# Optimization experiments

Hardware: AMD Instinct MI355X
Metric: run time of the kernel (lower is better)

Reference implementation:

```python
import jax, jax.numpy as jnp
import numpy as np

N_NODES = 50000
N_EDGES = 800000
D_NODE = 128
D_EDGE = 16
HID = 64
EPS = 1e-5


def _sage_conv(x, src, dst, Wl, bl, Wr, n_nodes):
    # PyG SAGEConv (mean aggr): out = lin_l(mean_{src->dst} x[src]) + lin_r(x)
    msg = x[src]                                        # [E, F] gather
    s = jax.ops.segment_sum(msg, dst, num_segments=n_nodes)   # [N, F]
    cnt = jax.ops.segment_sum(jnp.ones((src.shape[0],), x.dtype), dst,
                              num_segments=n_nodes)
    agg = s / jnp.maximum(cnt, 1.0)[:, None]
    return agg @ Wl.T + bl + x @ Wr.T


def _batchnorm(h, gamma, beta):
    # training-mode BN over node dim (biased variance, as in torch)
    mu = jnp.mean(h, axis=0)
    var = jnp.mean((h - mu) ** 2, axis=0)
    return gamma * (h - mu) / jnp.sqrt(var + EPS) + beta


def setup_inputs() -> dict:
    key = jax.random.key(0)
    ks = jax.random.split(key, 16)
    def lin(k, out_f, in_f):
        lim = 1.0 / np.sqrt(in_f)
        return jax.random.uniform(k, (out_f, in_f), jnp.float32, -lim, lim)
    x = jax.random.normal(ks[0], (N_NODES, D_NODE), jnp.float32)
    edge_index = jax.random.randint(ks[1], (2, N_EDGES), 0, N_NODES, jnp.int64)
    edge_attr = jax.random.normal(ks[2], (N_EDGES, D_EDGE), jnp.float32)
    return {
        "x": x, "edge_index": edge_index, "edge_attr": edge_attr,
        # SAGEConv 1
        "W1l": lin(ks[3], HID, D_NODE), "b1l": jnp.zeros((HID,), jnp.float32),
        "W1r": lin(ks[4], HID, D_NODE),
        "g1": jnp.ones((HID,), jnp.float32), "be1": jnp.zeros((HID,), jnp.float32),
        # SAGEConv 2
        "W2l": lin(ks[5], HID, HID), "b2l": jnp.zeros((HID,), jnp.float32),
        "W2r": lin(ks[6], HID, HID),
        "g2": jnp.ones((HID,), jnp.float32), "be2": jnp.zeros((HID,), jnp.float32),
        # edge MLP: (2*HID + D_EDGE) -> 128 -> 64 -> 2
        "Wm1": lin(ks[7], 128, 2 * HID + D_EDGE), "bm1": jnp.zeros((128,), jnp.float32),
        "Wm2": lin(ks[8], 64, 128), "bm2": jnp.zeros((64,), jnp.float32),
        "Wm3": lin(ks[9], 2, 64), "bm3": jnp.zeros((2,), jnp.float32),
    }


def reference(x, edge_index, edge_attr,
              W1l, b1l, W1r, g1, be1,
              W2l, b2l, W2r, g2, be2,
              Wm1, bm1, Wm2, bm2, Wm3, bm3):
    src, dst = edge_index[0], edge_index[1]
    n = x.shape[0]
    h = _sage_conv(x, src, dst, W1l, b1l, W1r, n)
    h = jax.nn.relu(_batchnorm(h, g1, be1))          # dropout = identity (eval)
    h = _sage_conv(h, src, dst, W2l, b2l, W2r, n)
    h = jax.nn.relu(_batchnorm(h, g2, be2))
    edge_in = jnp.concatenate([h[src], edge_attr, h[dst]], axis=1)  # [E, 144]
    z = jax.nn.relu(edge_in @ Wm1.T + bm1)
    z = jax.nn.relu(z @ Wm2.T + bm2)
    return z @ Wm3.T + bm3                           # [E, 2] logits
```

## Files before the change

### kernel.cpp

```cpp
#include <hip/hip_runtime.h>
#include <hip/hip_fp16.h>


#define EPS 1e-5f

typedef _Float16 h8 __attribute__((ext_vector_type(8)));
typedef float f32x4 __attribute__((ext_vector_type(4)));

__global__ __launch_bounds__(256) void k_prep_hist(
    const float* __restrict__ W1l, const float* __restrict__ W1r,
    const float* __restrict__ b1l,
    const float* __restrict__ W2l, const float* __restrict__ W2r,
    const float* __restrict__ b2l,
    const float* __restrict__ Wm1, const float* __restrict__ Wm2,
    float* __restrict__ Wt1, float* __restrict__ Wt2,
    float* __restrict__ bias1, float* __restrict__ bias2,
    __half* __restrict__ W2B, __half* __restrict__ W1B,
    const int* __restrict__ dst, int* __restrict__ deg, int E, int prepBlocks) {
  if ((int)blockIdx.x >= prepBlocks) {
    int e = (blockIdx.x - prepBlocks) * 256 + threadIdx.x;
    if (e < E) atomicAdd(&deg[dst[e]], 1);
    return;
  }
  int idx = blockIdx.x * 256 + threadIdx.x;
  if (idx < 16384) {
    int k = idx >> 7, f = idx & 127;
    Wt1[idx] = (f < 64) ? W1l[f * 128 + k] : W1r[(f - 64) * 128 + k];
    return;
  }
  idx -= 16384;
  if (idx < 8192) {
    int k = idx >> 7, f = idx & 127;
    Wt2[idx] = (f < 64) ? W2l[f * 64 + k] : W2r[(f - 64) * 64 + k];
    return;
  }
  idx -= 8192;
  if (idx < 128) { bias1[idx] = (idx < 64) ? 0.f : b1l[idx - 64]; return; }
  idx -= 128;
  if (idx < 128) { bias2[idx] = (idx < 64) ? 0.f : b2l[idx - 64]; return; }
  idx -= 128;
  if (idx < 8192) {
    int j = idx & 7, l = (idx >> 3) & 63, f = idx >> 9;
    int kc = f >> 2, tt = f & 3;
    int col = 16 * tt + (l & 15);
    int k = 32 * kc + (l >> 4) * 8 + j;
    W2B[idx] = __float2half(Wm2[col * 128 + k]);
    return;
  }
  idx -= 8192;
  if (idx < 20480) {
    int j = idx & 7, l = (idx >> 3) & 63, f = idx >> 9;
    int kc = f >> 3, nc = f & 7;
    int k = 32 * kc + (l >> 4) * 8 + j;
    int n = 16 * nc + (l & 15);
    float w;
    if (k < 64)       w = Wm1[n * 144 + k];
    else if (k < 128) w = Wm1[n * 144 + 80 + (k - 64)];
    else if (k < 144) w = Wm1[n * 144 + 64 + (k - 128)];
    else              w = 0.f;
    W1B[idx] = __float2half(w);
    return;
  }
}

__global__ __launch_bounds__(1024) void k_scan(
    const int* __restrict__ deg, int* __restrict__ rowptr,
    int* __restrict__ cursor, int N) {
  __shared__ int wsum[16];
  __shared__ int carry;
  const int lane = threadIdx.x & 63;
  const int w    = threadIdx.x >> 6;
  if (threadIdx.x == 0) carry = 0;
  __syncthreads();
  for (int base = 0; base < N; base += 1024) {
    int i = base + threadIdx.x;
    int v = (i < N) ? deg[i] : 0;
    int incl = v;
#pragma unroll
    for (int off = 1; off < 64; off <<= 1) {
      int t = __shfl_up(incl, off);
      if (lane >= off) incl += t;
    }
    if (lane == 63) wsum[w] = incl;
    __syncthreads();
    if (w == 0) {
      int ws_ = (lane < 16) ? wsum[lane] : 0;
      int wincl = ws_;
#pragma unroll
      for (int off = 1; off < 16; off <<= 1) {
        int t = __shfl_up(wincl, off);
        if (lane >= off) wincl += t;
      }
      if (lane < 16) wsum[lane] = wincl;
    }
    __syncthreads();
    int woff = carry + (w > 0 ? wsum[w - 1] : 0);
    int excl = woff + incl - v;
    if (i < N) { rowptr[i] = excl; cursor[i] = excl; }
    int tot = wsum[15];
    __syncthreads();
    if (threadIdx.x == 0) carry += tot;
    __syncthreads();
  }
  if (threadIdx.x == 0) rowptr[N] = carry;
}

__global__ __launch_bounds__(256) void k_fill(
    const int* __restrict__ src, const int* __restrict__ dst,
    int* __restrict__ cursor, int* __restrict__ csr_src,
    int* __restrict__ csr_dst, int* __restrict__ csr_eid,
    int* __restrict__ pos, int E) {
  int e = blockIdx.x * 256 + threadIdx.x;
  if (e < E) {
    int d = dst[e];
    int p = atomicAdd(&cursor[d], 1);
    csr_src[p] = src[e];
    csr_dst[p] = d;
    csr_eid[p] = e;
    pos[e] = p;
  }
}

__global__ __launch_bounds__(256) void k_scatter_out(
    const float* __restrict__ out2, const int* __restrict__ pos,
    float* __restrict__ out, int E) {
  int e = blockIdx.x * 256 + threadIdx.x;
  if (e < E) {
    int p = pos[e];
    *(float2*)&out[(size_t)e * 2] = *(const float2*)&out2[(size_t)p * 2];
  }
}

template<int K, int MODE>
__global__ __launch_bounds__(256) void k_gemm(
    const float* __restrict__ X, const float* __restrict__ stats,
    const float* __restrict__ Wt, const float* __restrict__ bias,
    __half* __restrict__ outH, float* __restrict__ outF, int N, int Ftot) {
  __shared__ __align__(16) float Xs[32][68];
  __shared__ __align__(16) float Ws_[32][128];
  const int tid = threadIdx.x;
  const int tx  = tid & 15;
  const int ty  = tid >> 4;
  const int n0  = blockIdx.x * 64;
  float acc[4][8];
#pragma unroll
  for (int j = 0; j < 8; ++j) {
    float bv = bias[8 * tx + j];
#pragma unroll
    for (int i = 0; i < 4; ++i) acc[i][j] = bv;
  }
  for (int k0 = 0; k0 < K; k0 += 32) {
    __syncthreads();
#pragma unroll
    for (int l = 0; l < 2; ++l) {
      int idx = tid * 2 + l;
      int kq = idx & 7, n = idx >> 3;
      float4 xv = make_float4(0.f, 0.f, 0.f, 0.f);
      if (n0 + n < N) xv = *(const float4*)&X[(size_t)(n0 + n) * K + k0 + kq * 4];
      if (stats) {
        int kb = k0 + kq * 4;
        xv.x = fmaxf(xv.x * stats[128 + kb + 0] + stats[192 + kb + 0], 0.f);
        xv.y = fmaxf(xv.y * stats[128 + kb + 1] + stats[192 + kb + 1], 0.f);
        xv.z = fmaxf(xv.z * stats[128 + kb + 2] + stats[192 + kb + 2], 0.f);
        xv.w = fmaxf(xv.w * stats[128 + kb + 3] + stats[192 + kb + 3], 0.f);
      }
      Xs[kq * 4 + 0][n] = xv.x;
      Xs[kq * 4 + 1][n] = xv.y;
      Xs[kq * 4 + 2][n] = xv.z;
      Xs[kq * 4 + 3][n] = xv.w;
    }
#pragma unroll
    for (int l = 0; l < 4; ++l) {
      int idx = tid + l * 256;
      int kr = idx >> 5, fc = idx & 31;
      *(float4*)&Ws_[kr][fc * 4] =
          *(const float4*)&Wt[(size_t)(k0 + kr) * Ftot + fc * 4];
    }
    __syncthreads();
#pragma unroll
    for (int kk = 0; kk < 32; ++kk) {
      float4 a  = *(const float4*)&Xs[kk][4 * ty];
      float4 b0 = *(const float4*)&Ws_[kk][8 * tx];
      float4 b1 = *(const float4*)&Ws_[kk][8 * tx + 4];
      float aa[4] = {a.x, a.y, a.z, a.w};
      float bb[8] = {b0.x, b0.y, b0.z, b0.w, b1.x, b1.y, b1.z, b1.w};
#pragma unroll
      for (int i = 0; i < 4; ++i)
#pragma unroll
        for (int j = 0; j < 8; ++j) acc[i][j] += aa[i] * bb[j];
    }
  }
#pragma unroll
  for (int i = 0; i < 4; ++i) {
    int n = n0 + 4 * ty + i;
    if (n >= N) continue;
    if (tx < 8) {
      __half2 hh[4];
#pragma unroll
      for (int c = 0; c < 4; ++c)
        hh[c] = __floats2half2_rn(acc[i][2 * c], acc[i][2 * c + 1]);
      *(uint4*)&outH[(size_t)n * 64 + 8 * tx] = *(uint4*)hh;
    } else {
      float* cp = outF + (size_t)n * 64 + 8 * tx - 64;
      *(float4*)cp = make_float4(acc[i][0], acc[i][1], acc[i][2], acc[i][3]);
      *(float4*)(cp + 4) = make_float4(acc[i][4], acc[i][5], acc[i][6], acc[i][7]);
    }
  }
}

__global__ __launch_bounds__(256) void k_agg(
    const __half* __restrict__ qb, const float* __restrict__ pb,
    const int* __restrict__ rowptr, const int* __restrict__ csr_src,
    float* __restrict__ hpre, float* __restrict__ stats, int N) {
  __shared__ float red[512];
  const int tid  = threadIdx.x;
  const int w    = tid >> 6;
  const int lane = tid & 63;
  const int g    = lane >> 3, c = lane & 7;
  float lsum = 0.f, lsq = 0.f;
  const int wid = blockIdx.x * 4 + w;
  const int nw  = gridDim.x * 4;
  for (int n = wid; n < N; n += nw) {
    const int r0 = rowptr[n], r1 = rowptr[n + 1];
    float s[8] = {0.f, 0.f, 0.f, 0.f, 0.f, 0.f, 0.f, 0.f};
    for (int j = r0 + g; j < r1; j += 8) {
      int a = csr_src[j];
      uint4 rv = *(const uint4*)&qb[(size_t)a * 64 + 8 * c];
      const __half2* hp = (const __half2*)&rv;
#pragma unroll
      for (int q = 0; q < 4; ++q) {
        float2 f2 = __half22float2(hp[q]);
        s[2 * q]     += f2.x;
        s[2 * q + 1] += f2.y;
      }
    }
#pragma unroll
    for (int m = 8; m < 64; m <<= 1)
#pragma unroll
      for (int q = 0; q < 8; ++q) s[q] += __shfl_xor(s[q], m);
    float sv = s[0];
#pragma unroll
    for (int q = 1; q < 8; ++q) sv = (g == q) ? s[q] : sv;
    float cdeg = (float)(r1 - r0);
    cdeg = cdeg > 1.f ? cdeg : 1.f;
    const int f = 8 * c + g;
    float v = sv / cdeg + pb[(size_t)n * 64 + f];
    hpre[(size_t)n * 64 + f] = v;
    lsum += v;
    lsq  += v * v;
  }
  red[tid]       = lsum;
  red[256 + tid] = lsq;
  __syncthreads();
  if (tid < 64) {
    float ts = red[tid] + red[tid + 64] + red[tid + 128] + red[tid + 192];
    float tq = red[256 + tid] + red[256 + tid + 64] + red[256 + tid + 128] + red[256 + tid + 192];
    int f = 8 * (tid & 7) + (tid >> 3);
    atomicAdd(&stats[f], ts);
    atomicAdd(&stats[64 + f], tq);
  }
}

__global__ void k_finalize(float* stats, const float* __restrict__ g,
                           const float* __restrict__ be, int N) {
  int f = threadIdx.x;
  float inv_n = 1.0f / (float)N;
  float mean = stats[f] * inv_n;
  float var  = stats[64 + f] * inv_n - mean * mean;
  float s = g[f] * rsqrtf(var + EPS);
  stats[128 + f] = s;
  stats[192 + f] = be[f] - mean * s;
}

__global__ __launch_bounds__(256) void k_bn(
    const float* __restrict__ H1, const float* __restrict__ stats,
    __half* __restrict__ H2, int N) {
  int idx = blockIdx.x * 256 + threadIdx.x;
  if (idx >= N * 8) return;
  int n = idx >> 3, f8 = (idx & 7) * 8;
  float4 h0 = *(const float4*)&H1[(size_t)n * 64 + f8];
  float4 h1 = *(const float4*)&H1[(size_t)n * 64 + f8 + 4];
  const float* sc = stats + 128 + f8;
  const float* sh = stats + 192 + f8;
  __half2 hh[4];
  hh[0] = __floats2half2_rn(fmaxf(h0.x * sc[0] + sh[0], 0.f),
                            fmaxf(h0.y * sc[1] + sh[1], 0.f));
  hh[1] = __floats2half2_rn(fmaxf(h0.z * sc[2] + sh[2], 0.f),
                            fmaxf(h0.w * sc[3] + sh[3], 0.f));
  hh[2] = __floats2half2_rn(fmaxf(h1.x * sc[4] + sh[4], 0.f),
                            fmaxf(h1.y * sc[5] + sh[5], 0.f));
  hh[3] = __floats2half2_rn(fmaxf(h1.z * sc[6] + sh[6], 0.f),
                            fmaxf(h1.w * sc[7] + sh[7], 0.f));
  *(uint4*)&H2[(size_t)n * 64 + f8] = *(uint4*)hh;
}

__global__ __launch_bounds__(256, 2) void k_edge(
    const __half* __restrict__ H2, const float* __restrict__ attr,
    const int* __restrict__ csrc, const int* __restrict__ cdst,
    const int* __restrict__ ceid,
    const __half* __restrict__ W1Bws, const __half* __restrict__ W2Bws,
    const float* __restrict__ bm1, const float* __restrict__ bm2,
    const float* __restrict__ Wm3, const float* __restrict__ bm3,
    float* __restrict__ out2, int E) {
  __shared__ __align__(16) _Float16 W1B[20480];
  __shared__ __align__(16) _Float16 W2B[8192];
  __shared__ __align__(16) _Float16 Z1f[64 * 136];

  const int tid  = threadIdx.x;
  const int lane = tid & 63;
  const int w    = tid >> 6;
  const int ln15 = lane & 15;
  const int quad = lane >> 4;

  for (int i = tid; i < 2560; i += 256)
    ((uint4*)W1B)[i] = ((const uint4*)W1Bws)[i];
  for (int i = tid; i < 1024; i += 256)
    ((uint4*)W2B)[i] = ((const uint4*)W2Bws)[i];

  float bm1v[8];
#pragma unroll
  for (int nc = 0; nc < 8; ++nc) bm1v[nc] = bm1[16 * nc + ln15];
  float bmv[4], w30[4], w31[4];
#pragma unroll
  for (int t = 0; t < 4; ++t) {
    bmv[t] = bm2[16 * t + ln15];
    w30[t] = Wm3[16 * t + ln15];
    w31[t] = Wm3[64 + 16 * t + ln15];
  }
  const float bm30 = bm3[0], bm31 = bm3[1];
  __syncthreads();

  const int nt = (E + 63) >> 6;
  const int G  = gridDim.x;
  const int rowoff = 16 * w + ln15;
  const int t0 = blockIdx.x;

#define ATTR_FRAG(EID, AF)                                                   \
  {                                                                          \
    AF = (h8){0, 0, 0, 0, 0, 0, 0, 0};                                       \
    if (quad < 2) {                                                          \
      float4 f0_ = *(const float4*)&attr[(size_t)(EID) * 16 + 8 * quad];     \
      float4 f1_ = *(const float4*)&attr[(size_t)(EID) * 16 + 8 * quad + 4]; \
      AF[0] = (_Float16)f0_.x; AF[1] = (_Float16)f0_.y;                      \
      AF[2] = (_Float16)f0_.z; AF[3] = (_Float16)f0_.w;                      \
      AF[4] = (_Float16)f1_.x; AF[5] = (_Float16)f1_.y;                      \
      AF[6] = (_Float16)f1_.z; AF[7] = (_Float16)f1_.w;                      \
    }                                                                        \
  }

  int s1, d1, e1i;
  h8 af0, af1, af2, af3, af4;
  {
    int er = (t0 << 6) + rowoff;
    if (er >= E) er = E - 1;
    int s = csrc[er], d = cdst[er], ei_ = ceid[er];
    af0 = *(const h8*)&H2[(size_t)s * 64 + 8 * quad];
    af1 = *(const h8*)&H2[(size_t)s * 64 + 32 + 8 * quad];
    af2 = *(const h8*)&H2[(size_t)d * 64 + 8 * quad];
    af3 = *(const h8*)&H2[(size_t)d * 64 + 32 + 8 * quad];
    ATTR_FRAG(ei_, af4);
  }
  {
    int er = ((t0 + G) << 6) + rowoff;
    if (er >= E) er = E - 1;
    s1 = csrc[er]; d1 = cdst[er]; e1i = ceid[er];
  }

  for (int t = t0; t < nt; t += G) {
    h8 nf0 = *(const h8*)&H2[(size_t)s1 * 64 + 8 * quad];
    h8 nf1 = *(const h8*)&H2[(size_t)s1 * 64 + 32 + 8 * quad];
    h8 nf2 = *(const h8*)&H2[(size_t)d1 * 64 + 8 * quad];
    h8 nf3 = *(const h8*)&H2[(size_t)d1 * 64 + 32 + 8 * quad];

    f32x4 acc1[8];
#pragma unroll
    for (int nc = 0; nc < 8; ++nc)
      acc1[nc] = (f32x4){bm1v[nc], bm1v[nc], bm1v[nc], bm1v[nc]};
#pragma unroll
    for (int nc = 0; nc < 8; ++nc)
      acc1[nc] = __builtin_amdgcn_mfma_f32_16x16x32_f16(
          af0, *(const h8*)&W1B[((0 * 8 + nc) << 9) + (lane << 3)], acc1[nc], 0, 0, 0);
#pragma unroll
    for (int nc = 0; nc < 8; ++nc)
      acc1[nc] = __builtin_amdgcn_mfma_f32_16x16x32_f16(
          af1, *(const h8*)&W1B[((1 * 8 + nc) << 9) + (lane << 3)], acc1[nc], 0, 0, 0);
#pragma unroll
    for (int nc = 0; nc < 8; ++nc)
      acc1[nc] = __builtin_amdgcn_mfma_f32_16x16x32_f16(
          af2, *(const h8*)&W1B[((2 * 8 + nc) << 9) + (lane << 3)], acc1[nc], 0, 0, 0);
#pragma unroll
    for (int nc = 0; nc < 8; ++nc)
      acc1[nc] = __builtin_amdgcn_mfma_f32_16x16x32_f16(
          af3, *(const h8*)&W1B[((3 * 8 + nc) << 9) + (lane << 3)], acc1[nc], 0, 0, 0);
#pragma unroll
    for (int nc = 0; nc < 8; ++nc)
      acc1[nc] = __builtin_amdgcn_mfma_f32_16x16x32_f16(
          af4, *(const h8*)&W1B[((4 * 8 + nc) << 9) + (lane << 3)], acc1[nc], 0, 0, 0);

    h8 nf4;
    ATTR_FRAG(e1i, nf4);
    int s2, d2, e2i;
    {
      int er = ((t + 2 * G) << 6) + rowoff;
      if (er >= E) er = E - 1;
      s2 = csrc[er]; d2 = cdst[er]; e2i = ceid[er];
    }

    const int ebase = 16 * w + 4 * quad;
#pragma unroll
    for (int nc = 0; nc < 8; ++nc)
#pragma unroll
      for (int r = 0; r < 4; ++r)
        Z1f[(ebase + r) * 136 + 16 * nc + ln15] =
            (_Float16)fmaxf(acc1[nc][r], 0.f);

    f32x4 acc2[4];
#pragma unroll
    for (int tt = 0; tt < 4; ++tt)
      acc2[tt] = (f32x4){bmv[tt], bmv[tt], bmv[tt], bmv[tt]};
#pragma unroll
    for (int kc = 0; kc < 4; ++kc) {
      h8 a = *(const h8*)&Z1f[(16 * w + ln15) * 136 + 32 * kc + 8 * quad];
#pragma unroll
      for (int tt = 0; tt < 4; ++tt) {
        h8 bf = *(const h8*)&W2B[((kc * 4 + tt) * 64 + lane) * 8];
        acc2[tt] = __builtin_amdgcn_mfma_f32_16x16x32_f16(a, bf, acc2[tt], 0, 0, 0);
      }
    }

    float p0[4], p1[4];
#pragma unroll
    for (int r = 0; r < 4; ++r) { p0[r] = 0.f; p1[r] = 0.f; }
#pragma unroll
    for (int tt = 0; tt < 4; ++tt)
#pragma unroll
      for (int r = 0; r < 4; ++r) {
        float z = fmaxf(acc2[tt][r], 0.f);
        p0[r] += z * w30[tt];
        p1[r] += z * w31[tt];
      }
#pragma unroll
    for (int r = 0; r < 4; ++r) {
#pragma unroll
      for (int m = 1; m < 16; m <<= 1) {
        p0[r] += __shfl_xor(p0[r], m);
        p1[r] += __shfl_xor(p1[r], m);
      }
      if (ln15 == 0) {
        int j = (t << 6) + 16 * w + 4 * quad + r;
        if (j < E)
          *(float2*)&out2[(size_t)j * 2] = make_float2(p0[r] + bm30, p1[r] + bm31);
      }
    }

    af0 = nf0; af1 = nf1; af2 = nf2; af3 = nf3; af4 = nf4;
    s1 = s2; d1 = d2; e1i = e2i;
  }
#undef ATTR_FRAG
}

extern "C" void kernel_launch(void* const* d_in, const int* in_sizes, int n_in,
                              void* d_out, int out_size, void* d_ws, size_t ws_size,
                              hipStream_t stream) {
  const float* x    = (const float*)d_in[0];
  const int*   ei   = (const int*)d_in[1];
  const float* attr = (const float*)d_in[2];
  const float* W1l  = (const float*)d_in[3];
  const float* b1l  = (const float*)d_in[4];
  const float* W1r  = (const float*)d_in[5];
  const float* g1   = (const float*)d_in[6];
  const float* be1  = (const float*)d_in[7];
  const float* W2l  = (const float*)d_in[8];
  const float* b2l  = (const float*)d_in[9];
  const float* W2r  = (const float*)d_in[10];
  const float* g2   = (const float*)d_in[11];
  const float* be2  = (const float*)d_in[12];
  const float* Wm1  = (const float*)d_in[13];
  const float* bm1  = (const float*)d_in[14];
  const float* Wm2  = (const float*)d_in[15];
  const float* bm2  = (const float*)d_in[16];
  const float* Wm3  = (const float*)d_in[17];
  const float* bm3  = (const float*)d_in[18];
  float* out = (float*)d_out;

  const int N = in_sizes[0] / 128;
  const int E = in_sizes[1] / 2;
  const int* srcI = ei;
  const int* dstI = ei + E;

  float* ws = (float*)d_ws;
  const size_t NF = (size_t)N * 64;
  float*  P32 = ws;
  float*  H1  = ws + NF;
  __half* Q16 = (__half*)(ws + 2 * NF);
  float* small  = ws + 2 * NF + NF / 2;
  float* stats1 = small;
  float* stats2 = stats1 + 256;
  float* Wt1    = stats2 + 256;
  float* Wt2    = Wt1 + 16384;
  float* bias1  = Wt2 + 8192;
  float* bias2  = bias1 + 128;
  __half* W1B   = (__half*)(bias2 + 128);
  __half* W2B   = (__half*)(bias2 + 128 + 10240);
  int* rowptr = (int*)(bias2 + 128 + 10240 + 4096);
  int* cursor = rowptr + (N + 1);
  int* deg    = cursor + N;
  int* csrsrc = deg + N;
  int* csrdst = csrsrc + E;
  int* csreid = csrdst + E;
  int* pos    = csreid + E;

  __half* H2  = Q16;
  float* out2 = H1;

  hipMemsetAsync(deg, 0, (size_t)N * sizeof(int), stream);
  hipMemsetAsync(stats1, 0, 512 * sizeof(float), stream);

  const int eBlocks = (E + 255) / 256;
  const int prepBlocks = (53504 + 255) / 256;
  k_prep_hist<<<prepBlocks + eBlocks, 256, 0, stream>>>(
      W1l, W1r, b1l, W2l, W2r, b2l, Wm1, Wm2,
      Wt1, Wt2, bias1, bias2, W2B, W1B,
      dstI, deg, E, prepBlocks);
  k_scan<<<1, 1024, 0, stream>>>(deg, rowptr, cursor, N);
  k_fill<<<eBlocks, 256, 0, stream>>>(srcI, dstI, cursor, csrsrc, csrdst,
                                      csreid, pos, E);

  const int mTiles = (N + 63) / 64;

  k_gemm<128, 0><<<mTiles, 256, 0, stream>>>(x, nullptr, Wt1, bias1, Q16, P32, N, 128);
  k_agg<<<1024, 256, 0, stream>>>(Q16, P32, rowptr, csrsrc, H1, stats1, N);
  k_finalize<<<1, 64, 0, stream>>>(stats1, g1, be1, N);

  k_gemm<64, 0><<<mTiles, 256, 0, stream>>>(H1, stats1, Wt2, bias2, Q16, P32, N, 128);
  k_agg<<<1024, 256, 0, stream>>>(Q16, P32, rowptr, csrsrc, H1, stats2, N);
  k_finalize<<<1, 64, 0, stream>>>(stats2, g2, be2, N);

  k_bn<<<(N * 8 + 255) / 256, 256, 0, stream>>>(H1, stats2, H2, N);

  k_edge<<<1024, 256, 0, stream>>>(H2, attr, csrsrc, csrdst, csreid,
                                   W1B, W2B, bm1, bm2, Wm3, bm3, out2, E);
  k_scatter_out<<<eBlocks, 256, 0, stream>>>(out2, pos, out, E);
}
```

Before: 597.0 us.

## Permute edge attributes to CSR order in fp16 during fill; drop edge prefetch

k_fill now converts edge_attr to fp16 and writes it in CSR-sorted order, so k_edge reads attributes contiguously by CSR position instead of through a gathered edge-id array. This removes the csr_eid array and the random fp32 attribute gather in the edge kernel. It also removes the software-pipelined prefetch of the next tile's node features and indices, which lowers register pressure but gives up some latency hiding. k_fill now does extra scattered 32-byte writes per edge.

```diff
diff --git a/kernel.cpp b/kernel.cpp
--- a/kernel.cpp
+++ b/kernel.cpp
@@ -107,17 +107,33 @@
 
 __global__ __launch_bounds__(256) void k_fill(
     const int* __restrict__ src, const int* __restrict__ dst,
+    const float* __restrict__ attr,
     int* __restrict__ cursor, int* __restrict__ csr_src,
-    int* __restrict__ csr_dst, int* __restrict__ csr_eid,
-    int* __restrict__ pos, int E) {
+    int* __restrict__ csr_dst, int* __restrict__ pos,
+    __half* __restrict__ attrC, int E) {
   int e = blockIdx.x * 256 + threadIdx.x;
   if (e < E) {
     int d = dst[e];
     int p = atomicAdd(&cursor[d], 1);
     csr_src[p] = src[e];
     csr_dst[p] = d;
-    csr_eid[p] = e;
     pos[e] = p;
+    const float4* at4 = (const float4*)attr;
+    float4 a0 = at4[(size_t)e * 4 + 0];
+    float4 a1 = at4[(size_t)e * 4 + 1];
+    float4 a2 = at4[(size_t)e * 4 + 2];
+    float4 a3 = at4[(size_t)e * 4 + 3];
+    __half2 hh[8];
+    hh[0] = __floats2half2_rn(a0.x, a0.y);
+    hh[1] = __floats2half2_rn(a0.z, a0.w);
+    hh[2] = __floats2half2_rn(a1.x, a1.y);
+    hh[3] = __floats2half2_rn(a1.z, a1.w);
+    hh[4] = __floats2half2_rn(a2.x, a2.y);
+    hh[5] = __floats2half2_rn(a2.z, a2.w);
+    hh[6] = __floats2half2_rn(a3.x, a3.y);
+    hh[7] = __floats2half2_rn(a3.z, a3.w);
+    *(uint4*)&attrC[(size_t)p * 16]     = *(uint4*)&hh[0];
+    *(uint4*)&attrC[(size_t)p * 16 + 8] = *(uint4*)&hh[4];
   }
 }
 
@@ -295,9 +311,8 @@
 }
 
 __global__ __launch_bounds__(256, 2) void k_edge(
-    const __half* __restrict__ H2, const float* __restrict__ attr,
+    const __half* __restrict__ H2, const __half* __restrict__ attrC,
     const int* __restrict__ csrc, const int* __restrict__ cdst,
-    const int* __restrict__ ceid,
     const __half* __restrict__ W1Bws, const __half* __restrict__ W2Bws,
     const float* __restrict__ bm1, const float* __restrict__ bm2,
     const float* __restrict__ Wm3, const float* __restrict__ bm3,
@@ -331,46 +346,21 @@
   __syncthreads();
 
   const int nt = (E + 63) >> 6;
-  const int G  = gridDim.x;
   const int rowoff = 16 * w + ln15;
-  const int t0 = blockIdx.x;
-
-#define ATTR_FRAG(EID, AF)                                                   \
-  {                                                                          \
-    AF = (h8){0, 0, 0, 0, 0, 0, 0, 0};                                       \
-    if (quad < 2) {                                                          \
-      float4 f0_ = *(const float4*)&attr[(size_t)(EID) * 16 + 8 * quad];     \
-      float4 f1_ = *(const float4*)&attr[(size_t)(EID) * 16 + 8 * quad + 4]; \
-      AF[0] = (_Float16)f0_.x; AF[1] = (_Float16)f0_.y;                      \
-      AF[2] = (_Float16)f0_.z; AF[3] = (_Float16)f0_.w;                      \
-      AF[4] = (_Float16)f1_.x; AF[5] = (_Float16)f1_.y;                      \
-      AF[6] = (_Float16)f1_.z; AF[7] = (_Float16)f1_.w;                      \
-    }                                                                        \
-  }
-
-  int s1, d1, e1i;
-  h8 af0, af1, af2, af3, af4;
-  {
-    int er = (t0 << 6) + rowoff;
+
+  for (int t = blockIdx.x; t < nt; t += gridDim.x) {
+    int er = (t << 6) + rowoff;
     if (er >= E) er = E - 1;
-    int s = csrc[er], d = cdst[er], ei_ = ceid[er];
-    af0 = *(const h8*)&H2[(size_t)s * 64 + 8 * quad];
-    af1 = *(const h8*)&H2[(size_t)s * 64 + 32 + 8 * quad];
-    af2 = *(const h8*)&H2[(size_t)d * 64 + 8 * quad];
-    af3 = *(const h8*)&H2[(size_t)d * 64 + 32 + 8 * quad];
-    ATTR_FRAG(ei_, af4);
-  }
-  {
-    int er = ((t0 + G) << 6) + rowoff;
-    if (er >= E) er = E - 1;
-    s1 = csrc[er]; d1 = cdst[er]; e1i = ceid[er];
-  }
-
-  for (int t = t0; t < nt; t += G) {
-    h8 nf0 = *(const h8*)&H2[(size_t)s1 * 64 + 8 * quad];
-    h8 nf1 = *(const h8*)&H2[(size_t)s1 * 64 + 32 + 8 * quad];
-    h8 nf2 = *(const h8*)&H2[(size_t)d1 * 64 + 8 * quad];
-    h8 nf3 = *(const h8*)&H2[(size_t)d1 * 64 + 32 + 8 * quad];
+    const int s = csrc[er];
+    const int d = cdst[er];
+
+    h8 af0 = *(const h8*)&H2[(size_t)s * 64 + 8 * quad];
+    h8 af1 = *(const h8*)&H2[(size_t)s * 64 + 32 + 8 * quad];
+    h8 af2 = *(const h8*)&H2[(size_t)d * 64 + 8 * quad];
+    h8 af3 = *(const h8*)&H2[(size_t)d * 64 + 32 + 8 * quad];
+    h8 af4 = (h8){0, 0, 0, 0, 0, 0, 0, 0};
+    if (quad < 2)
+      af4 = *(const h8*)&attrC[(size_t)er * 16 + 8 * quad];
 
     f32x4 acc1[8];
 #pragma unroll
@@ -396,15 +386,6 @@
     for (int nc = 0; nc < 8; ++nc)
       acc1[nc] = __builtin_amdgcn_mfma_f32_16x16x32_f16(
           af4, *(const h8*)&W1B[((4 * 8 + nc) << 9) + (lane << 3)], acc1[nc], 0, 0, 0);
-
-    h8 nf4;
-    ATTR_FRAG(e1i, nf4);
-    int s2, d2, e2i;
-    {
-      int er = ((t + 2 * G) << 6) + rowoff;
-      if (er >= E) er = E - 1;
-      s2 = csrc[er]; d2 = cdst[er]; e2i = ceid[er];
-    }
 
     const int ebase = 16 * w + 4 * quad;
 #pragma unroll
@@ -452,11 +433,7 @@
           *(float2*)&out2[(size_t)j * 2] = make_float2(p0[r] + bm30, p1[r] + bm31);
       }
     }
-
-    af0 = nf0; af1 = nf1; af2 = nf2; af3 = nf3; af4 = nf4;
-    s1 = s2; d1 = d2; e1i = e2i;
-  }
-#undef ATTR_FRAG
+  }
 }
 
 extern "C" void kernel_launch(void* const* d_in, const int* in_sizes, int n_in,
@@ -507,8 +484,8 @@
   int* deg    = cursor + N;
   int* csrsrc = deg + N;
   int* csrdst = csrsrc + E;
-  int* csreid = csrdst + E;
-  int* pos    = csreid + E;
+  int* pos    = csrdst + E;
+  __half* attrC = (__half*)(pos + E);
 
   __half* H2  = Q16;
   float* out2 = H1;
@@ -523,8 +500,8 @@
       Wt1, Wt2, bias1, bias2, W2B, W1B,
       dstI, deg, E, prepBlocks);
   k_scan<<<1, 1024, 0, stream>>>(deg, rowptr, cursor, N);
-  k_fill<<<eBlocks, 256, 0, stream>>>(srcI, dstI, cursor, csrsrc, csrdst,
-                                      csreid, pos, E);
+  k_fill<<<eBlocks, 256, 0, stream>>>(srcI, dstI, attr, cursor,
+                                      csrsrc, csrdst, pos, attrC, E);
 
   const int mTiles = (N + 63) / 64;
 
@@ -538,7 +515,7 @@
 
   k_bn<<<(N * 8 + 255) / 256, 256, 0, stream>>>(H1, stats2, H2, N);
 
-  k_edge<<<1024, 256, 0, stream>>>(H2, attr, csrsrc, csrdst, csreid,
+  k_edge<<<1024, 256, 0, stream>>>(H2, attrC, csrsrc, csrdst,
                                    W1B, W2B, bm1, bm2, Wm3, bm3, out2, E);
   k_scatter_out<<<eBlocks, 256, 0, stream>>>(out2, pos, out, E);
 }
```

Measured after the change: 567.9 us. -4.9%, faster.
